# Optimization experiments

Hardware: AMD Instinct MI355X
Metric: run time of the kernel (lower is better)

Reference implementation:

```python
import jax, jax.numpy as jnp
import numpy as np

N_NODES = 500_000   # users + items
N_USERS = 100_000
B = 2_000_000       # interactions in the batch
D = 64              # emb_size
SLOPE = 0.2         # leaky relu negative slope


def setup_inputs() -> dict:
    key = jax.random.key(0)
    ks = jax.random.split(key, 10)
    s = np.float32(1.0 / np.sqrt(D))
    E = jax.random.normal(ks[0], (N_NODES, D), jnp.float32) * s  # xavier-normal-ish
    W1a = jax.random.normal(ks[1], (D, D), jnp.float32) * s
    W2a = jax.random.normal(ks[2], (D, D), jnp.float32) * s
    W1b = jax.random.normal(ks[3], (D, D), jnp.float32) * s
    W2b = jax.random.normal(ks[4], (D, D), jnp.float32) * s
    W1c = jax.random.normal(ks[5], (D, D), jnp.float32) * s
    W2c = jax.random.normal(ks[6], (D, D), jnp.float32) * s
    users = jax.random.randint(ks[7], (B,), 0, N_USERS)
    pos = jax.random.randint(ks[8], (B,), N_USERS, N_NODES)
    neg = jax.random.randint(ks[9], (B,), N_USERS, N_NODES)
    return {"E": E, "W1a": W1a, "W2a": W2a, "W1b": W1b, "W2b": W2b,
            "W1c": W1c, "W2c": W2c, "users": users, "pos": pos, "neg": neg}


def _l2norm(x):
    # F.normalize(p=2, dim=1) with eps=1e-12
    return x / jnp.maximum(jnp.linalg.norm(x, axis=1, keepdims=True), 1e-12)


def reference(E, W1a, W2a, W1b, W2b, W1c, W2c, users, pos, neg):
    n = E.shape[0]
    # undirected edge list: user->item and item->user
    row = jnp.concatenate([users, pos])   # sources  [2B]
    col = jnp.concatenate([pos, users])   # targets  [2B]
    ones = jnp.ones(row.shape, E.dtype)
    deg = jax.ops.segment_sum(ones, col, num_segments=n)          # in-degree, no self loops
    deg_safe = jnp.where(deg > 0, deg, 1.0)
    dis = jnp.where(deg > 0, deg_safe ** -0.5, 0.0)
    norm1 = dis[row] * dis[col]                                    # [2B] neighbor norm

    self_idx = jnp.arange(n)
    src = jnp.concatenate([row, self_idx])                         # [2B+N] with self loops
    dst = jnp.concatenate([col, self_idx])
    dis_sl = (deg + 1.0) ** -0.5                                   # self loops add 1 everywhere
    norm2 = dis_sl[src] * dis_sl[dst]                              # [2B+N]
    norm1e = jnp.concatenate([norm1, jnp.zeros((n,), E.dtype)])    # interaction term off on self loops

    def layer(emb, W1, W2):
        x1 = emb @ W1.T                                            # [N,D]
        x2 = emb @ W2.T
        # per-edge message: norm_sl * W1 e_j + norm * (e_j * W2-side interaction)
        m = norm2[:, None] * x1[src] + norm1e[:, None] * (emb[src] * x2[dst])
        agg = jax.ops.segment_sum(m, dst, num_segments=n)          # scatter-add
        return _l2norm(jax.nn.leaky_relu(agg, SLOPE))              # dropout = identity (eval)

    e1 = layer(E, W1a, W2a)
    e2 = layer(e1, W1b, W2b)
    e3 = layer(e2, W1c, W2c)
    ef = jnp.concatenate([E, e1, e2, e3], axis=1)                  # pool='concat' -> [N,4D]

    u = ef[users]
    p = ef[pos]
    g = ef[neg]
    pos_sim = jnp.sum(u * p, axis=-1)
    neg_sim = jnp.sum(u * g, axis=-1)
    return pos_sim, neg_sim
```

## Files before the change

kernel.cpp:

```cpp
#include <hip/hip_runtime.h>
#include <hip/hip_bf16.h>


#define SCAN_B 1024

__device__ __forceinline__ float ld_e(const float* p) { return *p; }
__device__ __forceinline__ float ld_e(const __hip_bfloat16* p) { return __bfloat162float(*p); }
__device__ __forceinline__ void st_e(float* p, float v) { *p = v; }
__device__ __forceinline__ void st_e(__hip_bfloat16* p, float v) { *p = __float2bfloat16(v); }

__device__ __forceinline__ float bcastf(float x, int k) {
  return __uint_as_float((unsigned)__builtin_amdgcn_readlane(__float_as_uint(x), k));
}

__device__ __forceinline__ float4 ld4(const float* p) {
  return *reinterpret_cast<const float4*>(p);
}
__device__ __forceinline__ float4 ld4(const __hip_bfloat16* p) {
  ushort4 u = *reinterpret_cast<const ushort4*>(p);
  float4 r;
  r.x = __uint_as_float((unsigned)u.x << 16);
  r.y = __uint_as_float((unsigned)u.y << 16);
  r.z = __uint_as_float((unsigned)u.z << 16);
  r.w = __uint_as_float((unsigned)u.w << 16);
  return r;
}

__global__ void zero_i32(int* __restrict__ p, int n) {
  int i = blockIdx.x * blockDim.x + threadIdx.x;
  if (i < n) p[i] = 0;
}

__global__ void count_deg(const int* __restrict__ users, const int* __restrict__ pos,
                          int* __restrict__ deg, int b) {
  int i = blockIdx.x * blockDim.x + threadIdx.x;
  if (i < b) {
    atomicAdd(&deg[users[i]], 1);
    atomicAdd(&deg[pos[i]], 1);
  }
}

__global__ void scan1(const int* __restrict__ deg, int* __restrict__ tmp,
                      int* __restrict__ partial, int n) {
  __shared__ int sh[SCAN_B];
  int tid = threadIdx.x;
  int i = blockIdx.x * SCAN_B + tid;
  sh[tid] = (i < n) ? deg[i] : 0;
  __syncthreads();
  for (int off = 1; off < SCAN_B; off <<= 1) {
    int t = (tid >= off) ? sh[tid - off] : 0;
    __syncthreads();
    sh[tid] += t;
    __syncthreads();
  }
  if (i < n) tmp[i] = sh[tid];
  if (tid == SCAN_B - 1) partial[blockIdx.x] = sh[tid];
}

__global__ void scan2(int* __restrict__ partial, int g) {
  __shared__ int sh[SCAN_B];
  int tid = threadIdx.x;
  sh[tid] = (tid < g) ? partial[tid] : 0;
  __syncthreads();
  for (int off = 1; off < SCAN_B; off <<= 1) {
    int t = (tid >= off) ? sh[tid - off] : 0;
    __syncthreads();
    sh[tid] += t;
    __syncthreads();
  }
  if (tid < g) partial[tid] = sh[tid];
}

__global__ void scan3(const int* __restrict__ tmp, const int* __restrict__ partial,
                      const int* __restrict__ deg, int* __restrict__ rowptr,
                      int* __restrict__ cursor, int n) {
  int i = blockIdx.x * blockDim.x + threadIdx.x;
  if (i < n) {
    int blk = i >> 10;
    int off = blk > 0 ? partial[blk - 1] : 0;
    int incl = tmp[i] + off;
    rowptr[i + 1] = incl;
    cursor[i] = incl - deg[i];
    if (i == 0) rowptr[0] = 0;
  }
}

__global__ void compute_dd(const int* __restrict__ deg, float2* __restrict__ dd, int n) {
  int i = blockIdx.x * blockDim.x + threadIdx.x;
  if (i < n) {
    float d = (float)deg[i];
    float dis = deg[i] > 0 ? 1.0f / sqrtf(d) : 0.0f;
    float dsl = 1.0f / sqrtf(d + 1.0f);
    dd[i] = make_float2(dis, dsl);
  }
}

__global__ void fill_adj(const int* __restrict__ users, const int* __restrict__ pos,
                         int* __restrict__ cursor, int* __restrict__ adj, int b) {
  int i = blockIdx.x * blockDim.x + threadIdx.x;
  if (i < b) {
    int u = users[i], p = pos[i];
    adj[atomicAdd(&cursor[p], 1)] = u;
    adj[atomicAdd(&cursor[u], 1)] = p;
  }
}

template <typename SIN, typename SOUT>
__global__ void layer_fused(const SIN* __restrict__ e_in, const float* __restrict__ W1,
                            const float* __restrict__ W2, const int* __restrict__ rowptr,
                            const int* __restrict__ adj, const float2* __restrict__ dd,
                            SOUT* __restrict__ e_out, int n) {
  __shared__ float4 w1f4[1024];
  __shared__ float4 w2f4[1024];
  int tid = threadIdx.x;
  for (int i = tid; i < 1024; i += 512) {
    int m = i >> 6, d = i & 63;
    w1f4[i] = *reinterpret_cast<const float4*>(&W1[d * 64 + 4 * m]);
    w2f4[i] = *reinterpret_cast<const float4*>(&W2[d * 64 + 4 * m]);
  }
  __syncthreads();
  int lane = tid & 63;
  int wid = blockIdx.x * (blockDim.x >> 6) + (tid >> 6);
  if (wid >= n) return;
  int wu = __builtin_amdgcn_readfirstlane(wid);
  int rs = rowptr[wu], re = rowptr[wu + 1];
  float2 dd_i = dd[wu];
  float di = dd_i.x, dsl_i = dd_i.y;
  size_t base = (size_t)wu * 64 + lane;
  float ev = ld_e(&e_in[base]);
  float s1 = dsl_i * ev;
  float s2 = 0.0f;
  for (int e = rs; e < re; e += 8) {
    int m = re - e;
    int j[8];
    float2 w[8];
    float v[8];
#pragma unroll
    for (int q = 0; q < 8; ++q) {
      int idx = (q < m) ? (e + q) : rs;
      j[q] = adj[idx];
    }
#pragma unroll
    for (int q = 0; q < 8; ++q) w[q] = dd[j[q]];
#pragma unroll
    for (int q = 0; q < 8; ++q) v[q] = ld_e(&e_in[(size_t)j[q] * 64 + lane]);
#pragma unroll
    for (int q = 0; q < 8; ++q) {
      float ly = (q < m) ? w[q].y : 0.0f;
      float lx = (q < m) ? w[q].x : 0.0f;
      s1 = fmaf(ly, v[q], s1);
      s2 = fmaf(lx, v[q], s2);
    }
  }
  float t1 = 0.0f, t2 = 0.0f;
#pragma unroll
  for (int m = 0; m < 16; ++m) {
    float4 wa = w1f4[(m << 6) | lane];
    float4 wb = w2f4[(m << 6) | lane];
    int k = m << 2;
    t1 = fmaf(wa.x, bcastf(s1, k), t1);
    t2 = fmaf(wb.x, bcastf(ev, k), t2);
    t1 = fmaf(wa.y, bcastf(s1, k + 1), t1);
    t2 = fmaf(wb.y, bcastf(ev, k + 1), t2);
    t1 = fmaf(wa.z, bcastf(s1, k + 2), t1);
    t2 = fmaf(wb.z, bcastf(ev, k + 2), t2);
    t1 = fmaf(wa.w, bcastf(s1, k + 3), t1);
    t2 = fmaf(wb.w, bcastf(ev, k + 3), t2);
  }
  float agg = fmaf(dsl_i, t1, di * s2 * t2);
  float v = agg >= 0.0f ? agg : 0.2f * agg;
  float s = v * v;
#pragma unroll
  for (int m = 32; m; m >>= 1) s += __shfl_xor(s, m);
  float inv = 1.0f / fmaxf(sqrtf(s), 1e-12f);
  st_e(&e_out[base], v * inv);
}

template <typename ST>
__global__ void simk(const ST* __restrict__ ef, const int* __restrict__ users,
                     const int* __restrict__ pos, const int* __restrict__ neg,
                     float* __restrict__ out, int btot, int first) {
  int tid = blockIdx.x * blockDim.x + threadIdx.x;
  int q = tid & 15;
  int b = tid >> 4;
  if (b >= btot) return;
  int u = users[b], p = pos[b], g = neg[b];
  float4 eu = ld4(&ef[(size_t)u * 64 + q * 4]);
  float4 ep = ld4(&ef[(size_t)p * 64 + q * 4]);
  float4 eg = ld4(&ef[(size_t)g * 64 + q * 4]);
  float dp = eu.x * ep.x + eu.y * ep.y + eu.z * ep.z + eu.w * ep.w;
  float dn = eu.x * eg.x + eu.y * eg.y + eu.z * eg.z + eu.w * eg.w;
#pragma unroll
  for (int m = 8; m; m >>= 1) {
    dp += __shfl_xor(dp, m);
    dn += __shfl_xor(dn, m);
  }
  if (q == 0) {
    if (first) {
      out[b] = dp;
      out[btot + b] = dn;
    } else {
      out[b] += dp;
      out[btot + b] += dn;
    }
  }
}

template <typename ST>
static void run_pipeline(const float* E, const float* W1a, const float* W2a,
                         const float* W1b, const float* W2b, const float* W1c,
                         const float* W2c, const int* users, const int* pos,
                         const int* neg, float* out, void* d_ws, int N, int B,
                         hipStream_t stream) {
  size_t off = 0;
  auto alloc = [&](size_t bytes) -> void* {
    void* p = (char*)d_ws + off;
    off += (bytes + 255) & ~(size_t)255;
    return p;
  };
  int*    rowptr = (int*)alloc((size_t)(N + 1) * 4);
  int*    adj    = (int*)alloc((size_t)(2 * B) * 4);
  float2* dd     = (float2*)alloc((size_t)N * 8);
  ST*     eb0    = (ST*)alloc((size_t)N * 64 * sizeof(ST));
  ST*     eb1    = (ST*)alloc((size_t)N * 64 * sizeof(ST));
  char* tbase  = (char*)eb1;
  int* deg     = (int*)tbase;
  int* tmp     = (int*)(tbase + (size_t)N * 4);
  int* cursor  = (int*)(tbase + (size_t)N * 8);
  int* partial = (int*)(tbase + (size_t)N * 12);

  int gN = (N + 255) / 256;
  int gB = (B + 255) / 256;
  int G1 = (N + SCAN_B - 1) / SCAN_B;

  zero_i32<<<gN, 256, 0, stream>>>(deg, N);
  count_deg<<<gB, 256, 0, stream>>>(users, pos, deg, B);
  scan1<<<G1, SCAN_B, 0, stream>>>(deg, tmp, partial, N);
  scan2<<<1, SCAN_B, 0, stream>>>(partial, G1);
  scan3<<<gN, 256, 0, stream>>>(tmp, partial, deg, rowptr, cursor, N);
  compute_dd<<<gN, 256, 0, stream>>>(deg, dd, N);
  fill_adj<<<gB, 256, 0, stream>>>(users, pos, cursor, adj, B);

  int gw  = (N + 7) / 8;
  int gs  = (int)(((size_t)B * 16 + 255) / 256);

  simk<float><<<gs, 256, 0, stream>>>(E, users, pos, neg, out, B, 1);

  layer_fused<float, ST><<<gw, 512, 0, stream>>>(E, W1a, W2a, rowptr, adj, dd, eb0, N);
  simk<ST><<<gs, 256, 0, stream>>>(eb0, users, pos, neg, out, B, 0);

  layer_fused<ST, ST><<<gw, 512, 0, stream>>>(eb0, W1b, W2b, rowptr, adj, dd, eb1, N);
  simk<ST><<<gs, 256, 0, stream>>>(eb1, users, pos, neg, out, B, 0);

  layer_fused<ST, ST><<<gw, 512, 0, stream>>>(eb1, W1c, W2c, rowptr, adj, dd, eb0, N);
  simk<ST><<<gs, 256, 0, stream>>>(eb0, users, pos, neg, out, B, 0);
}

extern "C" void kernel_launch(void* const* d_in, const int* in_sizes, int n_in,
                              void* d_out, int out_size, void* d_ws, size_t ws_size,
                              hipStream_t stream) {
  const float* E   = (const float*)d_in[0];
  const float* W1a = (const float*)d_in[1];
  const float* W2a = (const float*)d_in[2];
  const float* W1b = (const float*)d_in[3];
  const float* W2b = (const float*)d_in[4];
  const float* W1c = (const float*)d_in[5];
  const float* W2c = (const float*)d_in[6];
  const int* users = (const int*)d_in[7];
  const int* pos   = (const int*)d_in[8];
  const int* neg   = (const int*)d_in[9];
  const int N = in_sizes[0] / 64;
  const int B = in_sizes[7];
  float* out = (float*)d_out;

  size_t fixed = (((size_t)(N + 1) * 4 + 255) & ~(size_t)255) +
                 (((size_t)(2 * B) * 4 + 255) & ~(size_t)255) +
                 (((size_t)N * 8 + 255) & ~(size_t)255);
  size_t need_f32 = fixed + 2 * ((((size_t)N * 64 * 4) + 255) & ~(size_t)255);

  if (ws_size >= need_f32) {
    run_pipeline<float>(E, W1a, W2a, W1b, W2b, W1c, W2c, users, pos, neg,
                        out, d_ws, N, B, stream);
  } else {
    run_pipeline<__hip_bfloat16>(E, W1a, W2a, W1b, W2b, W1c, W2c, users, pos,
                                 neg, out, d_ws, N, B, stream);
  }
}
```

Before: 2.874 ms.

## Merge similarity pass into layer kernel via interleaved block roles

Each layer launch now interleaves two block roles in groups of eight blocks. One role runs the graph aggregation layer, and the other computes the pos/neg similarity contribution of the previous layer's embeddings, which that launch reads as its input. The aim is to overlap the bandwidth-bound similarity gathers with the gather-heavy layer work and to drop three separate launches. The cost is a larger grid with early-exiting blocks, and similarity blocks that reserve the same 32KB of shared memory without using it, which may limit occupancy.

```diff
diff --git a/kernel.cpp b/kernel.cpp
--- a/kernel.cpp
+++ b/kernel.cpp
@@ -106,13 +106,49 @@
 }
 
 template <typename SIN, typename SOUT>
-__global__ void layer_fused(const SIN* __restrict__ e_in, const float* __restrict__ W1,
-                            const float* __restrict__ W2, const int* __restrict__ rowptr,
-                            const int* __restrict__ adj, const float2* __restrict__ dd,
-                            SOUT* __restrict__ e_out, int n) {
+__global__ void layer_sim(const SIN* __restrict__ e_in, const float* __restrict__ W1,
+                          const float* __restrict__ W2, const int* __restrict__ rowptr,
+                          const int* __restrict__ adj, const float2* __restrict__ dd,
+                          SOUT* __restrict__ e_out, int n,
+                          const int* __restrict__ users, const int* __restrict__ pos,
+                          const int* __restrict__ neg, float* __restrict__ out,
+                          int btot, int first) {
   __shared__ float4 w1f4[1024];
   __shared__ float4 w2f4[1024];
+  int bid = blockIdx.x;
+  int grp = bid >> 3;
+  int role = grp & 1;
+  int idx = ((grp >> 1) << 3) | (bid & 7);
   int tid = threadIdx.x;
+
+  if (role != 0) {
+    int b = idx * 32 + (tid >> 4);
+    if (b >= btot) return;
+    int q = tid & 15;
+    int u = users[b], p = pos[b], g = neg[b];
+    float4 eu = ld4(&e_in[(size_t)u * 64 + q * 4]);
+    float4 ep = ld4(&e_in[(size_t)p * 64 + q * 4]);
+    float4 eg = ld4(&e_in[(size_t)g * 64 + q * 4]);
+    float dp = eu.x * ep.x + eu.y * ep.y + eu.z * ep.z + eu.w * ep.w;
+    float dn = eu.x * eg.x + eu.y * eg.y + eu.z * eg.z + eu.w * eg.w;
+#pragma unroll
+    for (int m = 8; m; m >>= 1) {
+      dp += __shfl_xor(dp, m);
+      dn += __shfl_xor(dn, m);
+    }
+    if (q == 0) {
+      if (first) {
+        out[b] = dp;
+        out[btot + b] = dn;
+      } else {
+        out[b] += dp;
+        out[btot + b] += dn;
+      }
+    }
+    return;
+  }
+
+  if (idx * 8 >= n) return;
   for (int i = tid; i < 1024; i += 512) {
     int m = i >> 6, d = i & 63;
     w1f4[i] = *reinterpret_cast<const float4*>(&W1[d * 64 + 4 * m]);
@@ -120,7 +156,7 @@
   }
   __syncthreads();
   int lane = tid & 63;
-  int wid = blockIdx.x * (blockDim.x >> 6) + (tid >> 6);
+  int wid = idx * 8 + (tid >> 6);
   if (wid >= n) return;
   int wu = __builtin_amdgcn_readfirstlane(wid);
   int rs = rowptr[wu], re = rowptr[wu + 1];
@@ -137,8 +173,8 @@
     float v[8];
 #pragma unroll
     for (int q = 0; q < 8; ++q) {
-      int idx = (q < m) ? (e + q) : rs;
-      j[q] = adj[idx];
+      int idq = (q < m) ? (e + q) : rs;
+      j[q] = adj[idq];
     }
 #pragma unroll
     for (int q = 0; q < 8; ++q) w[q] = dd[j[q]];
@@ -241,19 +277,20 @@
   compute_dd<<<gN, 256, 0, stream>>>(deg, dd, N);
   fill_adj<<<gB, 256, 0, stream>>>(users, pos, cursor, adj, B);
 
-  int gw  = (N + 7) / 8;
-  int gs  = (int)(((size_t)B * 16 + 255) / 256);
-
-  simk<float><<<gs, 256, 0, stream>>>(E, users, pos, neg, out, B, 1);
-
-  layer_fused<float, ST><<<gw, 512, 0, stream>>>(E, W1a, W2a, rowptr, adj, dd, eb0, N);
-  simk<ST><<<gs, 256, 0, stream>>>(eb0, users, pos, neg, out, B, 0);
-
-  layer_fused<ST, ST><<<gw, 512, 0, stream>>>(eb0, W1b, W2b, rowptr, adj, dd, eb1, N);
-  simk<ST><<<gs, 256, 0, stream>>>(eb1, users, pos, neg, out, B, 0);
-
-  layer_fused<ST, ST><<<gw, 512, 0, stream>>>(eb1, W1c, W2c, rowptr, adj, dd, eb0, N);
-  simk<ST><<<gs, 256, 0, stream>>>(eb0, users, pos, neg, out, B, 0);
+  int gw = (N + 7) / 8;
+  int gs = (B + 31) / 32;
+  int npair = max(gw, gs);
+  int ngrp = (npair + 7) / 8;
+  int gm = 2 * ngrp * 8;
+  int gfin = (int)(((size_t)B * 16 + 255) / 256);
+
+  layer_sim<float, ST><<<gm, 512, 0, stream>>>(E, W1a, W2a, rowptr, adj, dd, eb0, N,
+                                               users, pos, neg, out, B, 1);
+  layer_sim<ST, ST><<<gm, 512, 0, stream>>>(eb0, W1b, W2b, rowptr, adj, dd, eb1, N,
+                                            users, pos, neg, out, B, 0);
+  layer_sim<ST, ST><<<gm, 512, 0, stream>>>(eb1, W1c, W2c, rowptr, adj, dd, eb0, N,
+                                            users, pos, neg, out, B, 0);
+  simk<ST><<<gfin, 256, 0, stream>>>(eb0, users, pos, neg, out, B, 0);
 }
 
 extern "C" void kernel_launch(void* const* d_in, const int* in_sizes, int n_in,
```

Result: slower. 3.485 ms (+21.2%).
